# Optimization experiments

Hardware: AMD Instinct MI355X
Metric: run time of the kernel (lower is better)

The kernel has to match this reference:

```python
import jax, jax.numpy as jnp
import numpy as np

B, S, R, L, Z = 2048, 277, 80, 12, 56


def setup_inputs() -> dict:
    key = jax.random.key(0)
    k0, k1, k2, k3, k4, k5 = jax.random.split(key, 6)
    true_idx = jax.random.randint(k0, (B, S), 0, R)
    x = jax.nn.one_hot(true_idx, R, dtype=jnp.float32)            # one-hot true rules
    recon_x = jax.nn.softmax(jax.random.normal(k1, (B, S, R)), axis=-1)  # post-softmax probs
    mu = jax.random.normal(k2, (B, Z), dtype=jnp.float32)
    log_var = jax.random.normal(k3, (B, Z), dtype=jnp.float32)
    ind_to_lhs_ind = jax.random.randint(k4, (R,), 0, L)
    masks = (jax.random.uniform(k5, (L, R)) > 0.5).astype(jnp.float32)
    # a valid grammar always allows the true rule under its own LHS mask
    masks = masks.at[ind_to_lhs_ind, jnp.arange(R)].set(1.0)
    return {"x": x, "recon_x": recon_x, "mu": mu, "log_var": log_var,
            "masks": masks, "ind_to_lhs_ind": ind_to_lhs_ind}


def reference(x, recon_x, mu, log_var, masks, ind_to_lhs_ind):
    batch_size, seq_len, n_rules = x.shape
    z_size = mu.shape[1]
    # apply_masks: fused gather + mask + renormalize (replaces B*S python loop)
    true_rule = jnp.argmax(x, axis=-1)                 # [B,S]
    mask = masks[ind_to_lhs_ind[true_rule]]            # [B,S,R]
    x_resc = recon_x * mask
    out = x_resc / jnp.sum(x_resc, axis=-1, keepdims=True)
    # BCELoss(size_average=False): torch clamps log terms at -100
    log_p = jnp.clip(jnp.log(out), -100.0, None)
    log_1mp = jnp.clip(jnp.log1p(-out), -100.0, None)
    bce = -jnp.sum(x * log_p + (1.0 - x) * log_1mp) / (seq_len * batch_size)
    # sample_z == False branch: moment-matching error
    avg_mu = jnp.sum(mu, axis=0) / batch_size          # [Z]
    var = jnp.matmul(mu.T, mu) / batch_size            # [Z,Z]
    var_err = var - jnp.eye(z_size, dtype=mu.dtype)
    mom_err = jnp.sum(avg_mu * avg_mu) / z_size + jnp.sum(jnp.abs(var_err)) / (z_size * z_size)
    return bce + mom_err
```

## Files before the change

kernel.cpp:

```cpp
#include <hip/hip_runtime.h>
#include <math.h>

#define Bn 2048
#define Sn 277
#define Rn 80
#define Ln 12
#define Zn 56
#define NROWS (Bn * Sn)
#define ROWS_PER_BLK 64
#define NBLK_BCE (NROWS / ROWS_PER_BLK)
#define NMOM 8
#define NBLK_TOT (NBLK_BCE + NMOM)

#define WS_CMASK 0
#define WS_BCE   1280
#define WS_VAR   72192
#define WS_AVG   172544

__global__ __launch_bounds__(256) void setup_kernel(
    const float* __restrict__ masks, const int* __restrict__ lhs, char* __restrict__ ws)
{
    unsigned* cmask_g = (unsigned*)(ws + WS_CMASK);
    for (int idx = threadIdx.x; idx < Rn * 4; idx += 256) {
        const int r = idx >> 2, w = idx & 3;
        unsigned bits = 0u;
        if (w < 3) {
            const int l = lhs[r];
            for (int b = 0; b < 32; ++b) {
                const int j = w * 32 + b;
                if (j < Rn && masks[l * Rn + j] > 0.5f) bits |= (1u << b);
            }
        }
        cmask_g[idx] = bits;
    }
}

__global__ __launch_bounds__(256) void main_kernel(
    const float* __restrict__ x, const float* __restrict__ recon,
    const float* __restrict__ mu, char* __restrict__ ws)
{
    const int tid = threadIdx.x;

    if (blockIdx.x >= NMOM) {
        const int bid = blockIdx.x - NMOM;
        __shared__ unsigned scmask[Rn * 4];
        __shared__ int samax[ROWS_PER_BLK];
        __shared__ float swsum[4];

        const unsigned* cmask_g = (const unsigned*)(ws + WS_CMASK);
        double* bce_partial = (double*)(ws + WS_BCE);

        scmask[tid] = cmask_g[tid];
        if (tid < Rn * 4 - 256) scmask[256 + tid] = cmask_g[256 + tid];

        const float4* xp = (const float4*)x + (size_t)bid * 1280;
        float4 x0 = xp[tid];
        float4 x1 = xp[tid + 256];
        float4 x2 = xp[tid + 512];
        float4 x3 = xp[tid + 768];
        float4 x4 = xp[tid + 1024];

        auto detect = [&](float4 v, int p) {
            int comp = -1;
            if (v.x > 0.5f) comp = 0;
            if (v.y > 0.5f) comp = 1;
            if (v.z > 0.5f) comp = 2;
            if (v.w > 0.5f) comp = 3;
            if (comp >= 0) {
                const int row = p / 20;
                const int f = p - row * 20;
                samax[row] = f * 4 + comp;
            }
        };
        detect(x0, tid);
        detect(x1, tid + 256);
        detect(x2, tid + 512);
        detect(x3, tid + 768);
        detect(x4, tid + 1024);
        __syncthreads();

        const int lrow = tid >> 2, c = tid & 3;
        const size_t row = (size_t)bid * ROWS_PER_BLK + lrow;
        const float4* rp = (const float4*)(recon + row * Rn);
        float4 m0 = rp[c];
        float4 m1 = rp[c + 4];
        float4 m2 = rp[c + 8];
        float4 m3 = rp[c + 12];
        float4 m4 = rp[c + 16];

        const int amax = samax[lrow];
        const unsigned u0 = scmask[amax * 4 + 0];
        const unsigned u1 = scmask[amax * 4 + 1];
        const unsigned u2 = scmask[amax * 4 + 2];
        const int sh = 4 * c;

        auto msk = [&](float4& v, unsigned u, int s) {
            v.x = ((u >> (s + 0)) & 1u) ? v.x : 0.f;
            v.y = ((u >> (s + 1)) & 1u) ? v.y : 0.f;
            v.z = ((u >> (s + 2)) & 1u) ? v.z : 0.f;
            v.w = ((u >> (s + 3)) & 1u) ? v.w : 0.f;
        };
        msk(m0, u0, sh);
        msk(m1, u0, sh + 16);
        msk(m2, u1, sh);
        msk(m3, u1, sh + 16);
        msk(m4, u2, sh);

        float d = ((m0.x + m0.y) + (m0.z + m0.w))
                + ((m1.x + m1.y) + (m1.z + m1.w))
                + ((m2.x + m2.y) + (m2.z + m2.w))
                + ((m3.x + m3.y) + (m3.z + m3.w))
                + ((m4.x + m4.y) + (m4.z + m4.w));
        d += __shfl_xor(d, 1);
        d += __shfl_xor(d, 2);
        const float invd = 1.0f / d;

        const int fa = amax >> 2;
        const int ca = fa & 3;
        const int ka = fa >> 2;
        const int comp = amax & 3;
        const bool owner = (c == ca);

        float ss = 0.0f;
        float ta = 1.0f;
        auto acc = [&](float4 v, int k) {
            const float t0 = fminf(v.x * invd, 1.f);
            const float t1 = fminf(v.y * invd, 1.f);
            const float t2 = fminf(v.z * invd, 1.f);
            const float t3 = fminf(v.w * invd, 1.f);
            ss += fmaxf(__logf(1.f - t0), -100.f);
            ss += fmaxf(__logf(1.f - t1), -100.f);
            ss += fmaxf(__logf(1.f - t2), -100.f);
            ss += fmaxf(__logf(1.f - t3), -100.f);
            if (owner && k == ka)
                ta = (comp == 0) ? t0 : (comp == 1) ? t1 : (comp == 2) ? t2 : t3;
        };
        acc(m0, 0); acc(m1, 1); acc(m2, 2); acc(m3, 3); acc(m4, 4);
        if (owner)
            ss += fmaxf(__logf(ta), -100.f) - fmaxf(__logf(1.f - ta), -100.f);

        float contrib = ss;
        #pragma unroll
        for (int o = 32; o; o >>= 1) contrib += __shfl_xor(contrib, o);
        if ((tid & 63) == 0) swsum[tid >> 6] = contrib;
        __syncthreads();
        if (tid == 0)
            bce_partial[bid] = (double)((swsum[0] + swsum[1]) + (swsum[2] + swsum[3]));
    } else {
        float* var_partial = (float*)(ws + WS_VAR);
        float* avg_partial = (float*)(ws + WS_AVG);
        __shared__ float sm[32 * Zn];

        const int m = blockIdx.x;
        float acc[13];
        #pragma unroll
        for (int k = 0; k < 13; ++k) acc[k] = 0.0f;
        float asum = 0.0f;

        for (int ch = 0; ch < 8; ++ch) {
            __syncthreads();
            const float* src = mu + ((size_t)m * 256 + ch * 32) * Zn;
            #pragma unroll
            for (int i = 0; i < 7; ++i) sm[tid + 256 * i] = src[tid + 256 * i];
            __syncthreads();

            #pragma unroll
            for (int k = 0; k < 13; ++k) {
                const int p = tid + 256 * k;
                if (p < Zn * Zn) {
                    const int i = p / Zn, j = p - i * Zn;
                    float a = 0.0f;
                    #pragma unroll 8
                    for (int r = 0; r < 32; ++r) a = fmaf(sm[r * Zn + i], sm[r * Zn + j], a);
                    acc[k] += a;
                }
            }
            if (tid < Zn) {
                float s = 0.0f;
                #pragma unroll 8
                for (int r = 0; r < 32; ++r) s += sm[r * Zn + tid];
                asum += s;
            }
        }
        #pragma unroll
        for (int k = 0; k < 13; ++k) {
            const int p = tid + 256 * k;
            if (p < Zn * Zn) var_partial[m * (Zn * Zn) + p] = acc[k];
        }
        if (tid < Zn) avg_partial[m * Zn + tid] = asum;
    }
}

__global__ __launch_bounds__(256) void finalize_kernel(
    const char* __restrict__ ws, float* __restrict__ out)
{
    const double* bce_partial = (const double*)(ws + WS_BCE);
    const float* var_partial = (const float*)(ws + WS_VAR);
    const float* avg_partial = (const float*)(ws + WS_AVG);
    __shared__ double sb[4];
    __shared__ float sv[4], sa[4];
    const int tid = threadIdx.x;

    double bsum = 0.0;
    for (int i = tid; i < NBLK_BCE; i += 256) bsum += bce_partial[i];

    float vsum = 0.0f;
    for (int p = tid; p < Zn * Zn; p += 256) {
        float v = 0.0f;
        #pragma unroll
        for (int m = 0; m < NMOM; ++m) v += var_partial[m * (Zn * Zn) + p];
        const int i = p / Zn, j = p - i * Zn;
        const float e = v * (1.0f / (float)Bn) - ((i == j) ? 1.0f : 0.0f);
        vsum += fabsf(e);
    }

    float asum = 0.0f;
    for (int z = tid; z < Zn; z += 256) {
        float a = 0.0f;
        #pragma unroll
        for (int m = 0; m < NMOM; ++m) a += avg_partial[m * Zn + z];
        asum += a * a;
    }

    #pragma unroll
    for (int o = 32; o; o >>= 1) {
        bsum += __shfl_xor(bsum, o);
        vsum += __shfl_xor(vsum, o);
        asum += __shfl_xor(asum, o);
    }
    if ((tid & 63) == 0) { const int w = tid >> 6; sb[w] = bsum; sv[w] = vsum; sa[w] = asum; }
    __syncthreads();
    if (tid == 0) {
        const double tb = (sb[0] + sb[1]) + (sb[2] + sb[3]);
        const double tv = (double)((sv[0] + sv[1]) + (sv[2] + sv[3]));
        const double ta = (double)((sa[0] + sa[1]) + (sa[2] + sa[3]));
        const double bce = -tb / ((double)Sn * (double)Bn);
        const double mom = ta / ((double)Bn * (double)Bn * (double)Zn)
                         + tv / ((double)Zn * (double)Zn);
        out[0] = (float)(bce + mom);
    }
}

extern "C" void kernel_launch(void* const* d_in, const int* in_sizes, int n_in,
                              void* d_out, int out_size, void* d_ws, size_t ws_size,
                              hipStream_t stream)
{
    const float* x     = (const float*)d_in[0];
    const float* recon = (const float*)d_in[1];
    const float* mu    = (const float*)d_in[2];
    const float* masks = (const float*)d_in[4];
    const int*   lhs   = (const int*)d_in[5];
    float* out = (float*)d_out;
    char* ws = (char*)d_ws;

    setup_kernel<<<1, 256, 0, stream>>>(masks, lhs, ws);
    main_kernel<<<NBLK_TOT, 256, 0, stream>>>(x, recon, mu, ws);
    finalize_kernel<<<1, 256, 0, stream>>>(ws, out);
}
```

Before: 383.2 us.

## Compute argmax per thread via weighted dot, drop shared-memory staging and syncs

The BCE path now has each quad of threads load its own row of x and recover the one-hot index with a weighted dot product reduced through DPP quad sums. This removes the shared-memory argmax table and both block barriers. The mask bits are pre-swizzled per thread column, and per-wave partials are written as floats. The moment blocks accumulate into global buffers with atomics, which needs an extra memset before launch. The argmax trick only works on exact one-hot inputs, and float atomics make the summation order nondeterministic.

```diff
diff --git a/kernel.cpp b/kernel.cpp
--- a/kernel.cpp
+++ b/kernel.cpp
@@ -11,27 +11,35 @@
 #define NBLK_BCE (NROWS / ROWS_PER_BLK)
 #define NMOM 8
 #define NBLK_TOT (NBLK_BCE + NMOM)
-
-#define WS_CMASK 0
-#define WS_BCE   1280
-#define WS_VAR   72192
-#define WS_AVG   172544
+#define NWAVE_BCE (NBLK_BCE * 4)
+
+#define WS_CM  0
+#define WS_BCE 1280
+#define WS_VAR 143104
+#define WS_AVG 155648
+
+__device__ __forceinline__ float qsum4(float v) {
+    int t = __builtin_amdgcn_update_dpp(0, __float_as_int(v), 0xB1, 0xF, 0xF, true);
+    v += __int_as_float(t);
+    t = __builtin_amdgcn_update_dpp(0, __float_as_int(v), 0x4E, 0xF, 0xF, true);
+    v += __int_as_float(t);
+    return v;
+}
 
 __global__ __launch_bounds__(256) void setup_kernel(
     const float* __restrict__ masks, const int* __restrict__ lhs, char* __restrict__ ws)
 {
-    unsigned* cmask_g = (unsigned*)(ws + WS_CMASK);
+    unsigned* cmask_sw = (unsigned*)(ws + WS_CM);
     for (int idx = threadIdx.x; idx < Rn * 4; idx += 256) {
-        const int r = idx >> 2, w = idx & 3;
+        const int r = idx >> 2, c = idx & 3;
+        const int l = lhs[r];
         unsigned bits = 0u;
-        if (w < 3) {
-            const int l = lhs[r];
-            for (int b = 0; b < 32; ++b) {
-                const int j = w * 32 + b;
-                if (j < Rn && masks[l * Rn + j] > 0.5f) bits |= (1u << b);
+        for (int k = 0; k < 5; ++k)
+            for (int comp = 0; comp < 4; ++comp) {
+                const int j = 16 * k + 4 * c + comp;
+                if (masks[l * Rn + j] > 0.5f) bits |= (1u << (4 * k + comp));
             }
-        }
-        cmask_g[idx] = bits;
+        cmask_sw[idx] = bits;
     }
 }
 
@@ -41,114 +49,9 @@
 {
     const int tid = threadIdx.x;
 
-    if (blockIdx.x >= NMOM) {
-        const int bid = blockIdx.x - NMOM;
-        __shared__ unsigned scmask[Rn * 4];
-        __shared__ int samax[ROWS_PER_BLK];
-        __shared__ float swsum[4];
-
-        const unsigned* cmask_g = (const unsigned*)(ws + WS_CMASK);
-        double* bce_partial = (double*)(ws + WS_BCE);
-
-        scmask[tid] = cmask_g[tid];
-        if (tid < Rn * 4 - 256) scmask[256 + tid] = cmask_g[256 + tid];
-
-        const float4* xp = (const float4*)x + (size_t)bid * 1280;
-        float4 x0 = xp[tid];
-        float4 x1 = xp[tid + 256];
-        float4 x2 = xp[tid + 512];
-        float4 x3 = xp[tid + 768];
-        float4 x4 = xp[tid + 1024];
-
-        auto detect = [&](float4 v, int p) {
-            int comp = -1;
-            if (v.x > 0.5f) comp = 0;
-            if (v.y > 0.5f) comp = 1;
-            if (v.z > 0.5f) comp = 2;
-            if (v.w > 0.5f) comp = 3;
-            if (comp >= 0) {
-                const int row = p / 20;
-                const int f = p - row * 20;
-                samax[row] = f * 4 + comp;
-            }
-        };
-        detect(x0, tid);
-        detect(x1, tid + 256);
-        detect(x2, tid + 512);
-        detect(x3, tid + 768);
-        detect(x4, tid + 1024);
-        __syncthreads();
-
-        const int lrow = tid >> 2, c = tid & 3;
-        const size_t row = (size_t)bid * ROWS_PER_BLK + lrow;
-        const float4* rp = (const float4*)(recon + row * Rn);
-        float4 m0 = rp[c];
-        float4 m1 = rp[c + 4];
-        float4 m2 = rp[c + 8];
-        float4 m3 = rp[c + 12];
-        float4 m4 = rp[c + 16];
-
-        const int amax = samax[lrow];
-        const unsigned u0 = scmask[amax * 4 + 0];
-        const unsigned u1 = scmask[amax * 4 + 1];
-        const unsigned u2 = scmask[amax * 4 + 2];
-        const int sh = 4 * c;
-
-        auto msk = [&](float4& v, unsigned u, int s) {
-            v.x = ((u >> (s + 0)) & 1u) ? v.x : 0.f;
-            v.y = ((u >> (s + 1)) & 1u) ? v.y : 0.f;
-            v.z = ((u >> (s + 2)) & 1u) ? v.z : 0.f;
-            v.w = ((u >> (s + 3)) & 1u) ? v.w : 0.f;
-        };
-        msk(m0, u0, sh);
-        msk(m1, u0, sh + 16);
-        msk(m2, u1, sh);
-        msk(m3, u1, sh + 16);
-        msk(m4, u2, sh);
-
-        float d = ((m0.x + m0.y) + (m0.z + m0.w))
-                + ((m1.x + m1.y) + (m1.z + m1.w))
-                + ((m2.x + m2.y) + (m2.z + m2.w))
-                + ((m3.x + m3.y) + (m3.z + m3.w))
-                + ((m4.x + m4.y) + (m4.z + m4.w));
-        d += __shfl_xor(d, 1);
-        d += __shfl_xor(d, 2);
-        const float invd = 1.0f / d;
-
-        const int fa = amax >> 2;
-        const int ca = fa & 3;
-        const int ka = fa >> 2;
-        const int comp = amax & 3;
-        const bool owner = (c == ca);
-
-        float ss = 0.0f;
-        float ta = 1.0f;
-        auto acc = [&](float4 v, int k) {
-            const float t0 = fminf(v.x * invd, 1.f);
-            const float t1 = fminf(v.y * invd, 1.f);
-            const float t2 = fminf(v.z * invd, 1.f);
-            const float t3 = fminf(v.w * invd, 1.f);
-            ss += fmaxf(__logf(1.f - t0), -100.f);
-            ss += fmaxf(__logf(1.f - t1), -100.f);
-            ss += fmaxf(__logf(1.f - t2), -100.f);
-            ss += fmaxf(__logf(1.f - t3), -100.f);
-            if (owner && k == ka)
-                ta = (comp == 0) ? t0 : (comp == 1) ? t1 : (comp == 2) ? t2 : t3;
-        };
-        acc(m0, 0); acc(m1, 1); acc(m2, 2); acc(m3, 3); acc(m4, 4);
-        if (owner)
-            ss += fmaxf(__logf(ta), -100.f) - fmaxf(__logf(1.f - ta), -100.f);
-
-        float contrib = ss;
-        #pragma unroll
-        for (int o = 32; o; o >>= 1) contrib += __shfl_xor(contrib, o);
-        if ((tid & 63) == 0) swsum[tid >> 6] = contrib;
-        __syncthreads();
-        if (tid == 0)
-            bce_partial[bid] = (double)((swsum[0] + swsum[1]) + (swsum[2] + swsum[3]));
-    } else {
-        float* var_partial = (float*)(ws + WS_VAR);
-        float* avg_partial = (float*)(ws + WS_AVG);
+    if (blockIdx.x < NMOM) {
+        float* var_g = (float*)(ws + WS_VAR);
+        float* avg_g = (float*)(ws + WS_AVG);
         __shared__ float sm[32 * Zn];
 
         const int m = blockIdx.x;
@@ -185,42 +88,116 @@
         #pragma unroll
         for (int k = 0; k < 13; ++k) {
             const int p = tid + 256 * k;
-            if (p < Zn * Zn) var_partial[m * (Zn * Zn) + p] = acc[k];
+            if (p < Zn * Zn) atomicAdd(&var_g[p], acc[k]);
         }
-        if (tid < Zn) avg_partial[m * Zn + tid] = asum;
-    }
+        if (tid < Zn) atomicAdd(&avg_g[tid], asum);
+        return;
+    }
+
+    const int bid = blockIdx.x - NMOM;
+    const unsigned* cmask_sw = (const unsigned*)(ws + WS_CM);
+    float* bce_partial = (float*)(ws + WS_BCE);
+
+    const int lrow = tid >> 2;
+    const int c = tid & 3;
+    const size_t row = (size_t)bid * ROWS_PER_BLK + lrow;
+    const float4* xp = (const float4*)(x + row * Rn);
+    const float4* rp = (const float4*)(recon + row * Rn);
+
+    const float4 xv0 = xp[c];
+    const float4 xv1 = xp[c + 4];
+    const float4 xv2 = xp[c + 8];
+    const float4 xv3 = xp[c + 12];
+    const float4 xv4 = xp[c + 16];
+    const float4 rv0 = rp[c];
+    const float4 rv1 = rp[c + 4];
+    const float4 rv2 = rp[c + 8];
+    const float4 rv3 = rp[c + 12];
+    const float4 rv4 = rp[c + 16];
+
+    auto dotc = [](const float4 v, float base) {
+        return fmaf(v.x, base, fmaf(v.y, base + 1.f, fmaf(v.z, base + 2.f, v.w * (base + 3.f))));
+    };
+    float dl = dotc(xv0, 0.f) + dotc(xv1, 16.f) + dotc(xv2, 32.f)
+             + dotc(xv3, 48.f) + dotc(xv4, 64.f);
+    const float xs = ((xv0.x + xv0.y) + (xv0.z + xv0.w)) + ((xv1.x + xv1.y) + (xv1.z + xv1.w))
+                   + ((xv2.x + xv2.y) + (xv2.z + xv2.w)) + ((xv3.x + xv3.y) + (xv3.z + xv3.w))
+                   + ((xv4.x + xv4.y) + (xv4.z + xv4.w));
+    dl = fmaf((float)(4 * c), xs, dl);
+    const int amax = (int)(qsum4(dl) + 0.5f);
+
+    const unsigned bits = cmask_sw[(amax << 2) | c];
+
+    auto mskd = [&](float4 v, int k) -> float4 {
+        float4 r;
+        r.x = ((bits >> (4 * k + 0)) & 1u) ? v.x : 0.f;
+        r.y = ((bits >> (4 * k + 1)) & 1u) ? v.y : 0.f;
+        r.z = ((bits >> (4 * k + 2)) & 1u) ? v.z : 0.f;
+        r.w = ((bits >> (4 * k + 3)) & 1u) ? v.w : 0.f;
+        return r;
+    };
+    const float4 m0 = mskd(rv0, 0);
+    const float4 m1 = mskd(rv1, 1);
+    const float4 m2 = mskd(rv2, 2);
+    const float4 m3 = mskd(rv3, 3);
+    const float4 m4 = mskd(rv4, 4);
+
+    float dd = ((m0.x + m0.y) + (m0.z + m0.w)) + ((m1.x + m1.y) + (m1.z + m1.w))
+             + ((m2.x + m2.y) + (m2.z + m2.w)) + ((m3.x + m3.y) + (m3.z + m3.w))
+             + ((m4.x + m4.y) + (m4.z + m4.w));
+    const float invd = __builtin_amdgcn_rcpf(qsum4(dd));
+
+    const int ka = amax >> 4;
+    const int ca = (amax >> 2) & 3;
+    const int comp = amax & 3;
+    const bool owner = (c == ca);
+
+    float ss = 0.0f;
+    float ta = 1.0f;
+    auto acc = [&](const float4 m, int k) {
+        const float t0 = fminf(m.x * invd, 1.f);
+        const float t1 = fminf(m.y * invd, 1.f);
+        const float t2 = fminf(m.z * invd, 1.f);
+        const float t3 = fminf(m.w * invd, 1.f);
+        ss += fmaxf(__logf(1.f - t0), -100.f) + fmaxf(__logf(1.f - t1), -100.f)
+            + fmaxf(__logf(1.f - t2), -100.f) + fmaxf(__logf(1.f - t3), -100.f);
+        if (owner && k == ka)
+            ta = (comp == 0) ? t0 : (comp == 1) ? t1 : (comp == 2) ? t2 : t3;
+    };
+    acc(m0, 0); acc(m1, 1); acc(m2, 2); acc(m3, 3); acc(m4, 4);
+    if (owner)
+        ss += fmaxf(__logf(ta), -100.f) - fmaxf(__logf(1.f - ta), -100.f);
+
+    ss = qsum4(ss);
+    ss += __shfl_xor(ss, 4);
+    ss += __shfl_xor(ss, 8);
+    ss += __shfl_xor(ss, 16);
+    ss += __shfl_xor(ss, 32);
+    if ((tid & 63) == 0)
+        bce_partial[bid * 4 + (tid >> 6)] = ss;
 }
 
 __global__ __launch_bounds__(256) void finalize_kernel(
     const char* __restrict__ ws, float* __restrict__ out)
 {
-    const double* bce_partial = (const double*)(ws + WS_BCE);
-    const float* var_partial = (const float*)(ws + WS_VAR);
-    const float* avg_partial = (const float*)(ws + WS_AVG);
+    const float* bce_partial = (const float*)(ws + WS_BCE);
+    const float* var_g = (const float*)(ws + WS_VAR);
+    const float* avg_g = (const float*)(ws + WS_AVG);
     __shared__ double sb[4];
     __shared__ float sv[4], sa[4];
     const int tid = threadIdx.x;
 
     double bsum = 0.0;
-    for (int i = tid; i < NBLK_BCE; i += 256) bsum += bce_partial[i];
+    for (int i = tid; i < NWAVE_BCE; i += 256) bsum += (double)bce_partial[i];
 
     float vsum = 0.0f;
     for (int p = tid; p < Zn * Zn; p += 256) {
-        float v = 0.0f;
-        #pragma unroll
-        for (int m = 0; m < NMOM; ++m) v += var_partial[m * (Zn * Zn) + p];
         const int i = p / Zn, j = p - i * Zn;
-        const float e = v * (1.0f / (float)Bn) - ((i == j) ? 1.0f : 0.0f);
+        const float e = var_g[p] * (1.0f / (float)Bn) - ((i == j) ? 1.0f : 0.0f);
         vsum += fabsf(e);
     }
-
     float asum = 0.0f;
-    for (int z = tid; z < Zn; z += 256) {
-        float a = 0.0f;
-        #pragma unroll
-        for (int m = 0; m < NMOM; ++m) a += avg_partial[m * Zn + z];
-        asum += a * a;
-    }
+    for (int z = tid; z < Zn; z += 256) { const float a = avg_g[z]; asum += a * a; }
 
     #pragma unroll
     for (int o = 32; o; o >>= 1) {
@@ -253,6 +230,7 @@
     float* out = (float*)d_out;
     char* ws = (char*)d_ws;
 
+    hipMemsetAsync(ws + WS_VAR, 0, 12544 + 224, stream);
     setup_kernel<<<1, 256, 0, stream>>>(masks, lhs, ws);
     main_kernel<<<NBLK_TOT, 256, 0, stream>>>(x, recon, mu, ws);
     finalize_kernel<<<1, 256, 0, stream>>>(ws, out);
```

Result: slower. 405.2 us (+5.7%).
